# Kernel optimization log

Measured on AMD Instinct MI355X. Metric: run time of the kernel, lower is better.

## Reference

```python
import jax, jax.numpy as jnp
import numpy as np

RX = (2, 9)
RY = (4, 9)
G, O = 64, 2          # column chunk size and overlap (hardcoded in original forward)
GK = RX[1]            # Gaussian (uniform box) kernel size, must be odd
M = N = 512


def _patches(x, kh, kw, pc, pr):
    # torch: F.pad(x,(pr,pr,pc,pc)).unfold(-2,kh,1).unfold(-2,kw,1).flatten(-2)
    xp = jnp.pad(x, ((0, 0), (0, 0), (pc, pc), (pr, pr)))
    p = jax.lax.conv_general_dilated_patches(xp, (kh, kw), (1, 1), 'VALID')  # (b, kh*kw, m, n) since c==1
    return jnp.moveaxis(p, 1, -1)[:, None]  # (b,1,m,n,kh*kw)


def _spatial_kernel(kh, kw):
    d = (jnp.arange(kh, dtype=jnp.float32) - kh // 2)[:, None] ** 2 \
        + (jnp.arange(kw, dtype=jnp.float32) - kw // 2)[None, :] ** 2
    return jnp.exp(-d.reshape(-1) / ((kh * kw) / 4.0) ** 2)


def _gen_weight(ych, kh, kw, pc, pr, sigma):
    p = _patches(ych, kh, kw, pc, pr)
    w = jnp.exp(-((p - ych[..., None]) ** 2) / (sigma / 2.0) ** 2)  # range (bilateral) term
    w = w * _spatial_kernel(kh, kw)                                  # spatial Gaussian term
    w = w * _patches(jnp.ones_like(ych), kh, kw, pc, pr)             # zero out padded taps
    return w / w.sum(-1, keepdims=True)


def _boxfilter(x, weight, kh, kw, pc, pr):
    return (_patches(x, kh, kw, pc, pr) * weight).sum(-1)


def _forward(X, y, r):
    sigma = r[0] * (y.max() - y.min())
    kh0, kw0, pc0, pr0 = 2 * RX[0] + 1, 2 * RY[0] + 1, RX[0], RY[0]  # detail kernel
    kh1, kw1, pc1, pr1 = 2 * RX[1] + 1, 2 * RY[1] + 1, RX[1], RY[1]  # base kernel
    gk = jnp.ones((1, 1, GK, GK), X.dtype) / float(GK * GK)
    pad = GK // 2
    conv = lambda z: jax.lax.conv_general_dilated(z, gk, (1, 1), [(pad, pad), (pad, pad)])

    # Angle = [0]: rotate(.,0,expand=True) and CenterCrop(m,n) are identities.
    XX, yy = X, y
    XXbase, yybase = conv(XX), conv(yy)
    XXdetail, yydetail = XX - XXbase, yy - yybase

    n = X.shape[-1]
    idx = np.arange(n)
    chunks = [idx[i:i + G] for i in range(0, n, G - O)]
    if len(chunks[-1]) <= 5:
        chunks[-2] = np.arange(chunks[-2][0], n)
        del chunks[-1]

    bdetail, Abase, bbase = [], [], []
    for index, ck in enumerate(chunks):
        s, e = int(ck[0]), int(ck[-1]) + 1
        Xb, Xd = XXbase[..., s:e], XXdetail[..., s:e]
        yb, yd = yybase[..., s:e], yydetail[..., s:e]
        wD = _gen_weight(Xd, kh0, kw0, pc0, pr0, sigma)
        wB = _gen_weight(Xb, kh1, kw1, pc1, pr1, sigma)
        lo = 0 if index == 0 else O // 2
        hi = None if index == len(chunks) - 1 else -(O // 2)
        bdetail.append(_boxfilter(yd - Xd, wD, kh0, kw0, pc0, pr0)[..., lo:hi])
        mean_y = _boxfilter(yb, wB, kh1, kw1, pc1, pr1)
        mean_x = _boxfilter(Xb, wB, kh1, kw1, pc1, pr1)
        var_x = _boxfilter(Xb * Xb, wB, kh1, kw1, pc1, pr1) - mean_x * mean_x
        cov_xy = _boxfilter(Xb * yb, wB, kh1, kw1, pc1, pr1) - mean_x * mean_y
        A = cov_xy / (var_x + 1e-6)
        b = mean_y - A * mean_x
        bbase.append(b[..., lo:hi])
        Abase.append(A[..., lo:hi])

    bdetail = jnp.concatenate(bdetail, -1)
    Abase = jnp.concatenate(Abase, -1)
    bbase = jnp.concatenate(bbase, -1)
    return Abase * XXbase + bbase + XXdetail + bdetail


def setup_inputs() -> dict:
    key = jax.random.key(0)
    k1, k2, k3 = jax.random.split(key, 3)
    X = jax.random.uniform(k1, (1, 1, M, N), dtype=jnp.float32)
    y = jax.random.uniform(k2, (1, 1, M, N), dtype=jnp.float32)
    r = jax.random.uniform(k3, (1,), dtype=jnp.float32)
    return {"X": X, "y": y, "r": r}


def reference(X, y, r):
    return _forward(X, y, r)
```

## Files before the change

kernel.cpp:

```cpp
#include <hip/hip_runtime.h>

#define W 512
#define NPIX (512*512)

typedef float v2f __attribute__((ext_vector_type(2)));

__device__ __forceinline__ float fexp2(float x) {
#if __has_builtin(__builtin_amdgcn_exp2f)
    return __builtin_amdgcn_exp2f(x);
#else
    return __expf(x * 0.6931471805599453f);
#endif
}
__device__ __forceinline__ v2f vfma(v2f a, v2f b, v2f c) {
    return __builtin_elementwise_fma(a, b, c);
}
__device__ __forceinline__ v2f bc2(float x) { v2f r; r.x = x; r.y = x; return r; }

__global__ __launch_bounds__(512) void k_prep(const float* __restrict__ X,
                                              const float* __restrict__ y,
                                              float2* __restrict__ XYb,
                                              float2* __restrict__ XDd,
                                              float2* __restrict__ partial) {
    __shared__ float sX[16][72], sY[16][72];
    __shared__ float rX[16][64], rY[16][64];
    __shared__ float wmn[8], wmx[8];
    int tx = threadIdx.x, ty = threadIdx.y;
    int t = ty * 64 + tx;
    int c0 = blockIdx.x * 64, r0 = blockIdx.y * 8;
    for (int i = t; i < 16 * 72; i += 512) {
        int rr = i / 72, cc = i - rr * 72;
        int gr = r0 - 4 + rr, gc = c0 - 4 + cc;
        bool ok = ((unsigned)gr < 512u) & ((unsigned)gc < 512u);
        sX[rr][cc] = ok ? X[gr * W + gc] : 0.f;
        sY[rr][cc] = ok ? y[gr * W + gc] : 0.f;
    }
    __syncthreads();
    for (int i = t; i < 16 * 64; i += 512) {
        int rr = i >> 6, cc = i & 63;
        float ax = 0.f, ay = 0.f;
#pragma unroll
        for (int j = 0; j < 9; ++j) { ax += sX[rr][cc + j]; ay += sY[rr][cc + j]; }
        rX[rr][cc] = ax; rY[rr][cc] = ay;
    }
    __syncthreads();
    float ax = 0.f, ay = 0.f;
#pragma unroll
    for (int j = 0; j < 9; ++j) { ax += rX[ty + j][tx]; ay += rY[ty + j][tx]; }
    const float inv81 = 1.0f / 81.0f;
    float xb = ax * inv81, yb = ay * inv81;
    float xv = sX[ty + 4][tx + 4], yv = sY[ty + 4][tx + 4];
    float xd = xv - xb;
    int p = (r0 + ty) * W + (c0 + tx);
    XYb[p] = make_float2(xb, yb);
    XDd[p] = make_float2(xd, (yv - yb) - xd);

    float mn = yv, mx = yv;
#pragma unroll
    for (int m = 32; m; m >>= 1) {
        mn = fminf(mn, __shfl_xor(mn, m));
        mx = fmaxf(mx, __shfl_xor(mx, m));
    }
    if (tx == 0) { wmn[ty] = mn; wmx[ty] = mx; }
    __syncthreads();
    if (t == 0) {
#pragma unroll
        for (int j = 1; j < 8; ++j) { mn = fminf(mn, wmn[j]); mx = fmaxf(mx, wmx[j]); }
        partial[blockIdx.y * 8 + blockIdx.x] = make_float2(mn, mx);
    }
}

__global__ __launch_bounds__(256) void k_main(const float2* __restrict__ XYb,
                                              const float2* __restrict__ XDd,
                                              const float2* __restrict__ partial,
                                              const float* __restrict__ r,
                                              float* __restrict__ out) {
    __shared__ float sbx[19];
    __shared__ float sdy[5];
    __shared__ float2 red[256];
    int tx = threadIdx.x, ty = threadIdx.y;
    int t = ty * 64 + tx;
    if (t < 19)      { int d = t - 9;      sbx[t]      = __expf(-(float)(d * d) / 8145.0625f); }
    else if (t < 24) { int d = t - 19 - 2; sdy[t - 19] = __expf(-(float)(d * d) / 126.5625f); }

    {
        float2 p0 = partial[t], p1 = partial[t + 256];
        red[t] = make_float2(fminf(p0.x, p1.x), fmaxf(p0.y, p1.y));
    }
    __syncthreads();
    for (int off = 128; off > 0; off >>= 1) {
        if (t < off) {
            red[t].x = fminf(red[t].x, red[t + off].x);
            red[t].y = fmaxf(red[t].y, red[t + off].y);
        }
        __syncthreads();
    }
    float sigma = r[0] * (red[0].y - red[0].x);
    float hh = 0.5f * sigma;
    float k2 = -1.4426950408889634f / (hh * hh);
    v2f k2v = bc2(k2);

    int c  = blockIdx.x * 64 + tx;
    int h0 = (blockIdx.y * 4 + ty) * 2;

    int chunk = (c == 0) ? 0 : (c - 1) / 62;
    if (chunk > 8) chunk = 8;
    int s = 62 * chunk;
    int e = (chunk == 8) ? 512 : (s + 64);

    const float ksb = -1.4426950408889634f / 8145.0625f;
    const float ksd = -1.4426950408889634f / 126.5625f;
    float cc[19];
#pragma unroll
    for (int j = 0; j < 19; ++j) {
        int nc = c - 9 + j, d = j - 9;
        cc[j] = ((nc >= s) & (nc < e)) ? ksb * (float)(d * d) : -1e30f;
    }
    float ccd[9];
#pragma unroll
    for (int j = 0; j < 9; ++j) {
        int nc = c - 4 + j, d = j - 4;
        ccd[j] = ((nc >= s) & (nc < e)) ? ksd * (float)(d * d) : -1e30f;
    }

    int p0 = h0 * W + c;
    v2f Xc2; Xc2.x = XYb[p0].x; Xc2.y = XYb[p0 + W].x;
    v2f Xd2; Xd2.x = XDd[p0].x; Xd2.y = XDd[p0 + W].x;

    v2f sw = bc2(0.f), swx = bc2(0.f), swy = bc2(0.f), swxx = bc2(0.f), swxy = bc2(0.f);
#pragma unroll 1
    for (int nh = h0 - 9; nh <= h0 + 10; ++nh) {
        if ((unsigned)nh >= 512u) continue;
        int dy0 = nh - h0;
        const float2* xr = XYb + (nh * W + c);
        v2f rs = bc2(0.f), rsx = bc2(0.f), rsy = bc2(0.f), rsxx = bc2(0.f), rsxy = bc2(0.f);
#pragma unroll
        for (int j = 0; j < 19; ++j) {
            float2 v = xr[j - 9];
            v2f xv = bc2(v.x), yv = bc2(v.y);
            v2f u = xv - Xc2;
            v2f a = vfma(u * k2v, u, bc2(cc[j]));
            v2f w; w.x = fexp2(a.x); w.y = fexp2(a.y);
            rs = rs + w;
            rsx = vfma(w, xv, rsx);
            rsy = vfma(w, yv, rsy);
            v2f tt = w * xv;
            rsxx = vfma(tt, xv, rsxx);
            rsxy = vfma(tt, yv, rsxy);
        }
        v2f ey;
        ey.x = (dy0 <= 9)  ? sbx[dy0 + 9] : 0.f;
        ey.y = (dy0 >= -8) ? sbx[dy0 + 8] : 0.f;
        sw   = vfma(ey, rs,   sw);
        swx  = vfma(ey, rsx,  swx);
        swy  = vfma(ey, rsy,  swy);
        swxx = vfma(ey, rsxx, swxx);
        swxy = vfma(ey, rsxy, swxy);
    }

    v2f swd = bc2(0.f), sv = bc2(0.f);
#pragma unroll 1
    for (int nh = h0 - 2; nh <= h0 + 3; ++nh) {
        if ((unsigned)nh >= 512u) continue;
        int dyd = nh - h0;
        const float2* dr = XDd + (nh * W + c);
        v2f rs = bc2(0.f), rv = bc2(0.f);
#pragma unroll
        for (int j = 0; j < 9; ++j) {
            float2 v = dr[j - 4];
            v2f xd = bc2(v.x), dv = bc2(v.y);
            v2f u = xd - Xd2;
            v2f a = vfma(u * k2v, u, bc2(ccd[j]));
            v2f w; w.x = fexp2(a.x); w.y = fexp2(a.y);
            rs = rs + w;
            rv = vfma(w, dv, rv);
        }
        v2f ey;
        ey.x = (dyd <= 2)  ? sdy[dyd + 2] : 0.f;
        ey.y = (dyd >= -1) ? sdy[dyd + 1] : 0.f;
        swd = vfma(ey, rs, swd);
        sv  = vfma(ey, rv, sv);
    }

    v2f inv; inv.x = 1.0f / sw.x; inv.y = 1.0f / sw.y;
    v2f mx = swx * inv, my = swy * inv;
    v2f varx = vfma(-mx, mx, swxx * inv);
    v2f cov  = vfma(-mx, my, swxy * inv);
    v2f A; A.x = cov.x / (varx.x + 1e-6f); A.y = cov.y / (varx.y + 1e-6f);
    v2f b = my - A * mx;
    v2f bd; bd.x = sv.x / swd.x; bd.y = sv.y / swd.y;
    v2f res = A * Xc2 + b + Xd2 + bd;
    out[p0]     = res.x;
    out[p0 + W] = res.y;
}

extern "C" void kernel_launch(void* const* d_in, const int* in_sizes, int n_in,
                              void* d_out, int out_size, void* d_ws, size_t ws_size,
                              hipStream_t stream) {
    const float* X = (const float*)d_in[0];
    const float* y = (const float*)d_in[1];
    const float* r = (const float*)d_in[2];
    float* out = (float*)d_out;
    float* wsf = (float*)d_ws;

    float2* partial = (float2*)(wsf + 64);
    float2* XYb = (float2*)(wsf + 4096) + 256;
    float2* XDd = XYb + NPIX + 512;

    k_prep<<<dim3(8, 64), dim3(64, 8), 0, stream>>>(X, y, XYb, XDd, partial);
    k_main<<<dim3(8, 64), dim3(64, 4), 0, stream>>>(XYb, XDd, partial, r, out);
}
```

Measured before the change: 92.46 us.

## Fuse box-filter prep into main kernel with LDS halo tiles, separate min/max pass

The min/max reduction of y moves into a small standalone kernel. The 9x9 box filter and detail computation are fused into the main bilateral kernel, which loads a 34x90 halo tile of X and y into LDS. It computes the separable box filter and detail values there, and reads all filter taps from LDS instead of global intermediates. This removes the global round-trip of the XYb/XDd intermediate buffers, in exchange for redundant halo computation and about 60KB of LDS per block, which limits occupancy.

```diff
diff --git a/kernel.cpp b/kernel.cpp
--- a/kernel.cpp
+++ b/kernel.cpp
@@ -1,7 +1,6 @@
 #include <hip/hip_runtime.h>
 
 #define W 512
-#define NPIX (512*512)
 
 typedef float v2f __attribute__((ext_vector_type(2)));
 
@@ -17,76 +16,50 @@
 }
 __device__ __forceinline__ v2f bc2(float x) { v2f r; r.x = x; r.y = x; return r; }
 
-__global__ __launch_bounds__(512) void k_prep(const float* __restrict__ X,
-                                              const float* __restrict__ y,
-                                              float2* __restrict__ XYb,
-                                              float2* __restrict__ XDd,
-                                              float2* __restrict__ partial) {
-    __shared__ float sX[16][72], sY[16][72];
-    __shared__ float rX[16][64], rY[16][64];
-    __shared__ float wmn[8], wmx[8];
+__global__ __launch_bounds__(256) void k_minmax(const float* __restrict__ y,
+                                                float2* __restrict__ partial) {
+    __shared__ float smn[256], smx[256];
+    int t = threadIdx.x;
+    const float4* y4 = (const float4*)y;
+    float4 v = y4[blockIdx.x * 256 + t];
+    float mn = fminf(fminf(v.x, v.y), fminf(v.z, v.w));
+    float mx = fmaxf(fmaxf(v.x, v.y), fmaxf(v.z, v.w));
+    smn[t] = mn; smx[t] = mx;
+    __syncthreads();
+    for (int off = 128; off > 0; off >>= 1) {
+        if (t < off) {
+            smn[t] = fminf(smn[t], smn[t + off]);
+            smx[t] = fmaxf(smx[t], smx[t + off]);
+        }
+        __syncthreads();
+    }
+    if (t == 0) partial[blockIdx.x] = make_float2(smn[0], smx[0]);
+}
+
+__global__ __launch_bounds__(256) void k_fused(const float* __restrict__ X,
+                                               const float* __restrict__ y,
+                                               const float2* __restrict__ partial,
+                                               const float* __restrict__ r,
+                                               float* __restrict__ out) {
+    __shared__ float sbx[19];
+    __shared__ float sdy[5];
+    __shared__ __align__(16) char ldsbuf[60256];
+    float*  sX  = (float*)ldsbuf;
+    float*  sY  = sX + 34 * 90;
+    float*  csX = sY + 34 * 90;
+    float*  csY = csX + 26 * 90;
+    float2* bXY = (float2*)(csY + 26 * 90);
+    float2* dXD = (float2*)csX;
+    float2* red = (float2*)sX;
+
     int tx = threadIdx.x, ty = threadIdx.y;
     int t = ty * 64 + tx;
     int c0 = blockIdx.x * 64, r0 = blockIdx.y * 8;
-    for (int i = t; i < 16 * 72; i += 512) {
-        int rr = i / 72, cc = i - rr * 72;
-        int gr = r0 - 4 + rr, gc = c0 - 4 + cc;
-        bool ok = ((unsigned)gr < 512u) & ((unsigned)gc < 512u);
-        sX[rr][cc] = ok ? X[gr * W + gc] : 0.f;
-        sY[rr][cc] = ok ? y[gr * W + gc] : 0.f;
-    }
-    __syncthreads();
-    for (int i = t; i < 16 * 64; i += 512) {
-        int rr = i >> 6, cc = i & 63;
-        float ax = 0.f, ay = 0.f;
-#pragma unroll
-        for (int j = 0; j < 9; ++j) { ax += sX[rr][cc + j]; ay += sY[rr][cc + j]; }
-        rX[rr][cc] = ax; rY[rr][cc] = ay;
-    }
-    __syncthreads();
-    float ax = 0.f, ay = 0.f;
-#pragma unroll
-    for (int j = 0; j < 9; ++j) { ax += rX[ty + j][tx]; ay += rY[ty + j][tx]; }
-    const float inv81 = 1.0f / 81.0f;
-    float xb = ax * inv81, yb = ay * inv81;
-    float xv = sX[ty + 4][tx + 4], yv = sY[ty + 4][tx + 4];
-    float xd = xv - xb;
-    int p = (r0 + ty) * W + (c0 + tx);
-    XYb[p] = make_float2(xb, yb);
-    XDd[p] = make_float2(xd, (yv - yb) - xd);
-
-    float mn = yv, mx = yv;
-#pragma unroll
-    for (int m = 32; m; m >>= 1) {
-        mn = fminf(mn, __shfl_xor(mn, m));
-        mx = fmaxf(mx, __shfl_xor(mx, m));
-    }
-    if (tx == 0) { wmn[ty] = mn; wmx[ty] = mx; }
-    __syncthreads();
-    if (t == 0) {
-#pragma unroll
-        for (int j = 1; j < 8; ++j) { mn = fminf(mn, wmn[j]); mx = fmaxf(mx, wmx[j]); }
-        partial[blockIdx.y * 8 + blockIdx.x] = make_float2(mn, mx);
-    }
-}
-
-__global__ __launch_bounds__(256) void k_main(const float2* __restrict__ XYb,
-                                              const float2* __restrict__ XDd,
-                                              const float2* __restrict__ partial,
-                                              const float* __restrict__ r,
-                                              float* __restrict__ out) {
-    __shared__ float sbx[19];
-    __shared__ float sdy[5];
-    __shared__ float2 red[256];
-    int tx = threadIdx.x, ty = threadIdx.y;
-    int t = ty * 64 + tx;
+
     if (t < 19)      { int d = t - 9;      sbx[t]      = __expf(-(float)(d * d) / 8145.0625f); }
     else if (t < 24) { int d = t - 19 - 2; sdy[t - 19] = __expf(-(float)(d * d) / 126.5625f); }
 
-    {
-        float2 p0 = partial[t], p1 = partial[t + 256];
-        red[t] = make_float2(fminf(p0.x, p1.x), fmaxf(p0.y, p1.y));
-    }
+    red[t] = partial[t];
     __syncthreads();
     for (int off = 128; off > 0; off >>= 1) {
         if (t < off) {
@@ -95,13 +68,54 @@
         }
         __syncthreads();
     }
-    float sigma = r[0] * (red[0].y - red[0].x);
+    float2 mm0 = red[0];
+    __syncthreads();
+    float sigma = r[0] * (mm0.y - mm0.x);
     float hh = 0.5f * sigma;
     float k2 = -1.4426950408889634f / (hh * hh);
     v2f k2v = bc2(k2);
 
+    for (int i = t; i < 34 * 90; i += 256) {
+        int rr = i / 90, cc2 = i - rr * 90;
+        int gr = r0 - 13 + rr, gc = c0 - 13 + cc2;
+        bool ok = ((unsigned)gr < 512u) & ((unsigned)gc < 512u);
+        float xv = 0.f, yv = 0.f;
+        if (ok) { xv = X[gr * W + gc]; yv = y[gr * W + gc]; }
+        sX[i] = xv; sY[i] = yv;
+    }
+    __syncthreads();
+
+    for (int i = t; i < 26 * 90; i += 256) {
+        int rr = i / 90, cc2 = i - rr * 90;
+        float ax = 0.f, ay = 0.f;
+#pragma unroll
+        for (int k = 0; k < 9; ++k) { ax += sX[(rr + k) * 90 + cc2]; ay += sY[(rr + k) * 90 + cc2]; }
+        csX[i] = ax; csY[i] = ay;
+    }
+    __syncthreads();
+
+    const float inv81 = 1.0f / 81.0f;
+    for (int i = t; i < 26 * 82; i += 256) {
+        int rr = i / 82, cc2 = i - rr * 82;
+        float ax = 0.f, ay = 0.f;
+#pragma unroll
+        for (int k = 0; k < 9; ++k) { ax += csX[rr * 90 + cc2 + k]; ay += csY[rr * 90 + cc2 + k]; }
+        bXY[i] = make_float2(ax * inv81, ay * inv81);
+    }
+    __syncthreads();
+
+    for (int i = t; i < 12 * 72; i += 256) {
+        int rr = i / 72, cc2 = i - rr * 72;
+        float2 b2 = bXY[(rr + 7) * 82 + (cc2 + 5)];
+        float xc = sX[(rr + 11) * 90 + (cc2 + 9)];
+        float yc = sY[(rr + 11) * 90 + (cc2 + 9)];
+        float xd = xc - b2.x;
+        dXD[i] = make_float2(xd, (yc - b2.y) - xd);
+    }
+    __syncthreads();
+
     int c  = blockIdx.x * 64 + tx;
-    int h0 = (blockIdx.y * 4 + ty) * 2;
+    int h0 = r0 + ty * 2;
 
     int chunk = (c == 0) ? 0 : (c - 1) / 62;
     if (chunk > 8) chunk = 8;
@@ -123,20 +137,21 @@
         ccd[j] = ((nc >= s) & (nc < e)) ? ksd * (float)(d * d) : -1e30f;
     }
 
-    int p0 = h0 * W + c;
-    v2f Xc2; Xc2.x = XYb[p0].x; Xc2.y = XYb[p0 + W].x;
-    v2f Xd2; Xd2.x = XDd[p0].x; Xd2.y = XDd[p0 + W].x;
+    v2f Xc2; Xc2.x = bXY[(2 * ty + 9)  * 82 + tx + 9].x;
+             Xc2.y = bXY[(2 * ty + 10) * 82 + tx + 9].x;
+    v2f Xd2; Xd2.x = dXD[(2 * ty + 2) * 72 + tx + 4].x;
+             Xd2.y = dXD[(2 * ty + 3) * 72 + tx + 4].x;
 
     v2f sw = bc2(0.f), swx = bc2(0.f), swy = bc2(0.f), swxx = bc2(0.f), swxy = bc2(0.f);
 #pragma unroll 1
     for (int nh = h0 - 9; nh <= h0 + 10; ++nh) {
         if ((unsigned)nh >= 512u) continue;
         int dy0 = nh - h0;
-        const float2* xr = XYb + (nh * W + c);
+        const float2* xr = bXY + (nh - r0 + 9) * 82 + tx;
         v2f rs = bc2(0.f), rsx = bc2(0.f), rsy = bc2(0.f), rsxx = bc2(0.f), rsxy = bc2(0.f);
 #pragma unroll
         for (int j = 0; j < 19; ++j) {
-            float2 v = xr[j - 9];
+            float2 v = xr[j];
             v2f xv = bc2(v.x), yv = bc2(v.y);
             v2f u = xv - Xc2;
             v2f a = vfma(u * k2v, u, bc2(cc[j]));
@@ -163,11 +178,11 @@
     for (int nh = h0 - 2; nh <= h0 + 3; ++nh) {
         if ((unsigned)nh >= 512u) continue;
         int dyd = nh - h0;
-        const float2* dr = XDd + (nh * W + c);
+        const float2* dr2 = dXD + (nh - r0 + 2) * 72 + tx;
         v2f rs = bc2(0.f), rv = bc2(0.f);
 #pragma unroll
         for (int j = 0; j < 9; ++j) {
-            float2 v = dr[j - 4];
+            float2 v = dr2[j];
             v2f xd = bc2(v.x), dv = bc2(v.y);
             v2f u = xd - Xd2;
             v2f a = vfma(u * k2v, u, bc2(ccd[j]));
@@ -190,6 +205,7 @@
     v2f b = my - A * mx;
     v2f bd; bd.x = sv.x / swd.x; bd.y = sv.y / swd.y;
     v2f res = A * Xc2 + b + Xd2 + bd;
+    int p0 = h0 * W + c;
     out[p0]     = res.x;
     out[p0 + W] = res.y;
 }
@@ -201,12 +217,8 @@
     const float* y = (const float*)d_in[1];
     const float* r = (const float*)d_in[2];
     float* out = (float*)d_out;
-    float* wsf = (float*)d_ws;
-
-    float2* partial = (float2*)(wsf + 64);
-    float2* XYb = (float2*)(wsf + 4096) + 256;
-    float2* XDd = XYb + NPIX + 512;
-
-    k_prep<<<dim3(8, 64), dim3(64, 8), 0, stream>>>(X, y, XYb, XDd, partial);
-    k_main<<<dim3(8, 64), dim3(64, 4), 0, stream>>>(XYb, XDd, partial, r, out);
-}
+    float2* partial = (float2*)d_ws;
+
+    k_minmax<<<256, 256, 0, stream>>>(y, partial);
+    k_fused<<<dim3(8, 64), dim3(64, 4), 0, stream>>>(X, y, partial, r, out);
+}
```

New measurement: 92.07 us. About the same (-0.4%).
